# Kernel optimization log

Measured on AMD Instinct MI355X. Metric: run time of the kernel, lower is better.

The kernel has to match this reference:

```python
import jax, jax.numpy as jnp
import numpy as np

B, C, H, W = 8, 512, 32, 32


def setup_inputs() -> dict:
    key = jax.random.key(0)
    kx, kq, kk, k6 = jax.random.split(key, 4)
    std = 0.02
    return {
        "x": jax.random.normal(kx, (B, C, H, W), dtype=jnp.float32),
        "Wq": jax.random.normal(kq, (C, C), dtype=jnp.float32) * std,
        "bq": jnp.zeros((C,), dtype=jnp.float32),
        "Wk": jax.random.normal(kk, (C, C), dtype=jnp.float32) * std,
        "bk": jnp.zeros((C,), dtype=jnp.float32),
        "W6": jax.random.normal(k6, (C, C), dtype=jnp.float32) * std,
        "b6": jnp.zeros((C,), dtype=jnp.float32),
    }


def reference(x, Wq, bq, Wk, bk, W6, b6):
    b, c, h, w = x.shape
    hw = h * w
    scale = 1.0 / (c ** 0.5)
    # [B, HW, C] token-major view of the feature map
    xf = jnp.transpose(x.reshape(b, c, hw), (0, 2, 1))
    # 1x1 convs are per-pixel linear layers (weight layout: [C_out, C_in])
    q = xf @ Wq.T + bq                      # [B, HW, C]
    k = xf @ Wk.T + bk                      # [B, HW, C]
    # cross-batch attention scores: every pixel attends to every pixel of every image
    scores = q.reshape(b * hw, c) @ k.reshape(b * hw, c).T   # [B*HW, B*HW]
    s = scores.reshape(b * hw, b, hw)
    # per-query: max response within each image, then mean over images
    xw = jnp.max(s, axis=-1).mean(axis=-1)  # [B*HW]
    xw = xw.reshape(b, hw) * scale
    xw = jax.nn.softmax(xw, axis=-1).reshape(b, 1, h, w)
    x5 = x * xw                             # spatial gating
    # final 1x1 conv
    of = jnp.transpose(x5.reshape(b, c, hw), (0, 2, 1)) @ W6.T + b6
    return jnp.transpose(of, (0, 2, 1)).reshape(b, c, h, w)
```

## Files before the change

### kernel.cpp

```cpp
#include <hip/hip_runtime.h>


typedef __attribute__((ext_vector_type(8))) short bf16x8;
typedef __attribute__((ext_vector_type(4))) float f32x4;
typedef __attribute__((ext_vector_type(2))) long long i64x2;

__device__ __forceinline__ unsigned short f2bf(float f) {
  unsigned u = __builtin_bit_cast(unsigned, f);
  u += 0x7FFFu + ((u >> 16) & 1u);
  return (unsigned short)(u >> 16);
}

__device__ __forceinline__ unsigned char f2e4m3(float x) {
  unsigned u = __builtin_bit_cast(unsigned, x);
  unsigned char s = (unsigned char)((u >> 24) & 0x80u);
  unsigned a = u & 0x7FFFFFFFu;
  if (a >= 0x43E00000u) return s | 0x7Eu;
  if (a < 0x3C800000u) {
    float q = __builtin_bit_cast(float, a) * 512.f;
    int m = (int)(q + 0.5f);
    return s | (unsigned char)m;
  }
  unsigned r = a + 0x7FFFFu + ((a >> 20) & 1u);
  int e = (int)((r >> 23) & 0xFF) - 127;
  if (e > 8) return s | 0x7Eu;
  unsigned m3 = (r >> 20) & 0x7u;
  return s | (unsigned char)(((e + 7) << 3) | m3);
}

__device__ __forceinline__ void gload_lds16(const void* g, void* l) {
  __builtin_amdgcn_global_load_lds(
      (const __attribute__((address_space(1))) unsigned int*)g,
      (__attribute__((address_space(3))) unsigned int*)l, 16, 0, 0);
}

__global__ __launch_bounds__(256) void prep(const float* __restrict__ x,
                                            const float* __restrict__ Wq,
                                            const float* __restrict__ Wk,
                                            const float* __restrict__ W6,
                                            short* __restrict__ xt,
                                            short* __restrict__ wcat) {
  const int bid = blockIdx.x, u = threadIdx.x;
  if (bid < 1024) {
    const int p0 = (bid & 15) * 64, c0 = ((bid >> 4) & 7) * 64, b = bid >> 7;
    __shared__ float t[64][65];
    {
      const int p4 = u & 15, cr = u >> 4;
      for (int cc = 0; cc < 4; ++cc) {
        const int c = cc * 16 + cr;
        const float4 v = *(const float4*)&x[((size_t)(b * 512 + c0 + c)) * 1024 + p0 + p4 * 4];
        t[p4 * 4 + 0][c] = v.x; t[p4 * 4 + 1][c] = v.y;
        t[p4 * 4 + 2][c] = v.z; t[p4 * 4 + 3][c] = v.w;
      }
    }
    __syncthreads();
    {
      const int c4 = u & 15, pr = u >> 4;
      for (int pp = 0; pp < 4; ++pp) {
        const int p = pp * 16 + pr;
        ushort4 o;
        o.x = f2bf(t[p][c4 * 4 + 0]); o.y = f2bf(t[p][c4 * 4 + 1]);
        o.z = f2bf(t[p][c4 * 4 + 2]); o.w = f2bf(t[p][c4 * 4 + 3]);
        *(ushort4*)&xt[((size_t)(b * 1024 + p0 + p)) * 512 + c0 + c4 * 4] = o;
      }
    }
  } else {
    const int i = (bid - 1024) * 256 + u;
    const int idx = i * 4;
    const float* src = (idx < 262144) ? Wq : (idx < 524288) ? Wk : W6;
    const float4 v = *(const float4*)&src[idx & 262143];
    ushort4 o;
    o.x = f2bf(v.x); o.y = f2bf(v.y); o.z = f2bf(v.z); o.w = f2bf(v.w);
    *(ushort4*)&wcat[idx] = o;
  }
}

__global__ __launch_bounds__(256) void gemm_qk(const short* __restrict__ xt,
                                               const short* __restrict__ wcat,
                                               const float* __restrict__ bq,
                                               const float* __restrict__ bk,
                                               unsigned char* __restrict__ qk8) {
  __shared__ short lds_a[128 * 64];
  __shared__ short lds_b[128 * 64];
  const int tid = threadIdx.x, w = tid >> 6, lane = tid & 63;
  const int wr = w >> 1, wc = w & 1;
  const int quad = lane >> 4, lcol = lane & 15;
  const int srow = lane & 15, skq = lane >> 4;
  const int m0 = blockIdx.x * 128, n0 = blockIdx.y * 128;

  f32x4 acc[4][4];
#pragma unroll
  for (int i = 0; i < 4; ++i)
#pragma unroll
    for (int j = 0; j < 4; ++j)
#pragma unroll
      for (int r = 0; r < 4; ++r) acc[i][j][r] = 0.f;

  const short* Abase = xt + (size_t)(m0 + srow) * 512 + skq * 8;
  const short* Bbase = wcat + (size_t)(n0 + srow) * 512 + skq * 8;

  for (int kt = 0; kt < 8; ++kt) {
    const int kb = kt * 64;
    __syncthreads();
#pragma unroll
    for (int gg = 0; gg < 2; ++gg) {
      const int g = w + gg * 4;
      gload_lds16(Abase + (size_t)(g * 16) * 512 + kb,      lds_a + g * 1024);
      gload_lds16(Abase + (size_t)(g * 16) * 512 + kb + 32, lds_a + g * 1024 + 512);
      gload_lds16(Bbase + (size_t)(g * 16) * 512 + kb,      lds_b + g * 1024);
      gload_lds16(Bbase + (size_t)(g * 16) * 512 + kb + 32, lds_b + g * 1024 + 512);
    }
    __syncthreads();
#pragma unroll
    for (int h = 0; h < 2; ++h) {
      bf16x8 af[4], bf[4];
#pragma unroll
      for (int i = 0; i < 4; ++i)
        af[i] = *(const bf16x8*)&lds_a[(wr * 4 + i) * 1024 + h * 512 + lane * 8];
#pragma unroll
      for (int j = 0; j < 4; ++j)
        bf[j] = *(const bf16x8*)&lds_b[(wc * 4 + j) * 1024 + h * 512 + lane * 8];
#pragma unroll
      for (int i = 0; i < 4; ++i)
#pragma unroll
        for (int j = 0; j < 4; ++j)
          acc[i][j] = __builtin_amdgcn_mfma_f32_16x16x32_bf16(af[i], bf[j], acc[i][j], 0, 0, 0);
    }
  }

  const float* bias = (blockIdx.y >= 4) ? bk : bq;
#pragma unroll
  for (int i = 0; i < 4; ++i)
#pragma unroll
    for (int j = 0; j < 4; ++j) {
      const int row = m0 + wr * 64 + i * 16 + quad * 4;
      const int col = n0 + wc * 64 + j * 16 + lcol;
      const float bv = bias[col & 511];
#pragma unroll
      for (int r = 0; r < 4; ++r)
        qk8[(size_t)(row + r) * 1024 + col] = f2e4m3(acc[i][j][r] + bv);
    }
}

__global__ __launch_bounds__(256) void gemm_scores(const unsigned char* __restrict__ qk8,
                                                   float* __restrict__ wsmx) {
  __shared__ unsigned char lds_a[8192];
  __shared__ unsigned char lds_b[8192];
  __shared__ float partial[128][2];
  const int tid = threadIdx.x, w = tid >> 6, lane = tid & 63;
  const int wr = w >> 1, wc = w & 1;
  const int quad = lane >> 4, lcol = lane & 15;
  const int skq = lane >> 4, srow = lane & 15;
  const int m0 = blockIdx.x * 128, n0 = blockIdx.y * 128;

  f32x4 acc[4][4];
#pragma unroll
  for (int i = 0; i < 4; ++i)
#pragma unroll
    for (int j = 0; j < 4; ++j)
#pragma unroll
      for (int r = 0; r < 4; ++r) acc[i][j][r] = 0.f;

  const unsigned char* Abase = qk8 + (size_t)(m0 + srow) * 1024 + skq * 16;
  const unsigned char* Bbase = qk8 + (size_t)(n0 + srow) * 1024 + 512 + skq * 16;

  for (int kt = 0; kt < 8; ++kt) {
    const int kb = kt * 64;
    __syncthreads();
    gload_lds16(Abase + (size_t)(w * 16) * 1024 + kb,       lds_a + w * 1024);
    gload_lds16(Abase + (size_t)((4 + w) * 16) * 1024 + kb, lds_a + (4 + w) * 1024);
    gload_lds16(Bbase + (size_t)(w * 16) * 1024 + kb,       lds_b + w * 1024);
    gload_lds16(Bbase + (size_t)((4 + w) * 16) * 1024 + kb, lds_b + (4 + w) * 1024);
    __syncthreads();
    i64x2 af[4], bf[4];
#pragma unroll
    for (int i = 0; i < 4; ++i) af[i] = *(const i64x2*)&lds_a[(wr * 4 + i) * 1024 + lane * 16];
#pragma unroll
    for (int j = 0; j < 4; ++j) bf[j] = *(const i64x2*)&lds_b[(wc * 4 + j) * 1024 + lane * 16];
#pragma unroll
    for (int i = 0; i < 4; ++i)
#pragma unroll
      for (int j = 0; j < 4; ++j) {
        acc[i][j] = __builtin_amdgcn_mfma_f32_16x16x32_fp8_fp8(af[i].x, bf[j].x, acc[i][j], 0, 0, 0);
        acc[i][j] = __builtin_amdgcn_mfma_f32_16x16x32_fp8_fp8(af[i].y, bf[j].y, acc[i][j], 0, 0, 0);
      }
  }

#pragma unroll
  for (int i = 0; i < 4; ++i) {
#pragma unroll
    for (int r = 0; r < 4; ++r) {
      float v = fmaxf(fmaxf(acc[i][0][r], acc[i][1][r]),
                      fmaxf(acc[i][2][r], acc[i][3][r]));
#pragma unroll
      for (int off = 1; off < 16; off <<= 1) v = fmaxf(v, __shfl_xor(v, off));
      if (lcol == 0) partial[wr * 64 + i * 16 + quad * 4 + r][wc] = v;
    }
  }
  __syncthreads();
  if (tid < 128)
    wsmx[(size_t)blockIdx.y * 8192 + m0 + tid] = fmaxf(partial[tid][0], partial[tid][1]);
}

__global__ __launch_bounds__(1024) void softmax_xw(const float* __restrict__ wsmx,
                                                   float* __restrict__ xw) {
  const int b = blockIdx.x, p = threadIdx.x;
  const int m = b * 1024 + p;
  float s = 0.f;
#pragma unroll
  for (int img = 0; img < 8; ++img) {
    float mx = -1e30f;
#pragma unroll
    for (int t = 0; t < 8; ++t) mx = fmaxf(mx, wsmx[(size_t)(img * 8 + t) * 8192 + m]);
    s += mx;
  }
  const float logit = s * 0.005524271728019903f;
  __shared__ float red[16];
  float v = logit;
#pragma unroll
  for (int off = 32; off >= 1; off >>= 1) v = fmaxf(v, __shfl_xor(v, off));
  if ((p & 63) == 0) red[p >> 6] = v;
  __syncthreads();
  float bmax = red[0];
#pragma unroll
  for (int t = 1; t < 16; ++t) bmax = fmaxf(bmax, red[t]);
  const float e = expf(logit - bmax);
  float sv = e;
#pragma unroll
  for (int off = 32; off >= 1; off >>= 1) sv += __shfl_xor(sv, off);
  __syncthreads();
  if ((p & 63) == 0) red[p >> 6] = sv;
  __syncthreads();
  float bsum = 0.f;
#pragma unroll
  for (int t = 0; t < 16; ++t) bsum += red[t];
  xw[m] = e / bsum;
}

__global__ __launch_bounds__(256) void gemm_out(const short* __restrict__ xt,
                                                const short* __restrict__ wcat,
                                                const float* __restrict__ xw,
                                                const float* __restrict__ b6,
                                                float* __restrict__ out) {
  __shared__ short lds_a[64 * 64];
  __shared__ short lds_b[64 * 64];
  const int tid = threadIdx.x, w = tid >> 6, lane = tid & 63;
  const int wr = w >> 1, wc = w & 1;
  const int quad = lane >> 4, lcol = lane & 15;
  const int srow = lane & 15, skq = lane >> 4;
  const int m0 = blockIdx.x * 64, n0 = blockIdx.y * 64;

  f32x4 acc[2][2];
#pragma unroll
  for (int i = 0; i < 2; ++i)
#pragma unroll
    for (int j = 0; j < 2; ++j)
#pragma unroll
      for (int r = 0; r < 4; ++r) acc[i][j][r] = 0.f;

  const short* Abase = xt + (size_t)(m0 + w * 16 + srow) * 512 + skq * 8;
  const short* Bbase = wcat + (size_t)(1024 + n0 + w * 16 + srow) * 512 + skq * 8;

  for (int kt = 0; kt < 8; ++kt) {
    const int kb = kt * 64;
    __syncthreads();
    gload_lds16(Abase + kb,      lds_a + w * 1024);
    gload_lds16(Abase + kb + 32, lds_a + w * 1024 + 512);
    gload_lds16(Bbase + kb,      lds_b + w * 1024);
    gload_lds16(Bbase + kb + 32, lds_b + w * 1024 + 512);
    __syncthreads();
#pragma unroll
    for (int h = 0; h < 2; ++h) {
      bf16x8 af[2], bf[2];
#pragma unroll
      for (int i = 0; i < 2; ++i)
        af[i] = *(const bf16x8*)&lds_a[(wr * 2 + i) * 1024 + h * 512 + lane * 8];
#pragma unroll
      for (int j = 0; j < 2; ++j)
        bf[j] = *(const bf16x8*)&lds_b[(wc * 2 + j) * 1024 + h * 512 + lane * 8];
#pragma unroll
      for (int i = 0; i < 2; ++i)
#pragma unroll
        for (int j = 0; j < 2; ++j)
          acc[i][j] = __builtin_amdgcn_mfma_f32_16x16x32_bf16(af[i], bf[j], acc[i][j], 0, 0, 0);
    }
  }

#pragma unroll
  for (int i = 0; i < 2; ++i) {
    const int mbase = m0 + wr * 32 + i * 16 + quad * 4;
    const int b = mbase >> 10, p = mbase & 1023;
    const float4 wv = *(const float4*)&xw[mbase];
#pragma unroll
    for (int j = 0; j < 2; ++j) {
      const int col = n0 + wc * 32 + j * 16 + lcol;
      const float bias = b6[col];
      float4 o;
      o.x = acc[i][j][0] * wv.x + bias;
      o.y = acc[i][j][1] * wv.y + bias;
      o.z = acc[i][j][2] * wv.z + bias;
      o.w = acc[i][j][3] * wv.w + bias;
      *(float4*)&out[((size_t)(b * 512 + col)) * 1024 + p] = o;
    }
  }
}

extern "C" void kernel_launch(void* const* d_in, const int* in_sizes, int n_in,
                              void* d_out, int out_size, void* d_ws, size_t ws_size,
                              hipStream_t stream) {
  const float* x  = (const float*)d_in[0];
  const float* Wq = (const float*)d_in[1];
  const float* bq = (const float*)d_in[2];
  const float* Wk = (const float*)d_in[3];
  const float* bk = (const float*)d_in[4];
  const float* W6 = (const float*)d_in[5];
  const float* b6 = (const float*)d_in[6];
  float* out = (float*)d_out;

  char* ws = (char*)d_ws;
  short* xt          = (short*)(ws + 0);
  short* wcat        = (short*)(ws + 8388608);
  unsigned char* qk8 = (unsigned char*)(ws + 10485760);
  float* wsmx        = (float*)(ws + 18874368);
  float* xw          = (float*)(ws + 20971520);

  prep<<<1792, 256, 0, stream>>>(x, Wq, Wk, W6, xt, wcat);
  gemm_qk<<<dim3(64, 8), 256, 0, stream>>>(xt, wcat, bq, bk, qk8);
  gemm_scores<<<dim3(64, 64), 256, 0, stream>>>(qk8, wsmx);
  softmax_xw<<<8, 1024, 0, stream>>>(wsmx, xw);
  gemm_out<<<dim3(128, 8), 256, 0, stream>>>(xt, wcat, xw, b6, out);
}
```

Before: 194.5 us.

## Restructure score GEMM: per-wave 32-row strips, A in registers, larger K chunks

The FP8 score GEMM now gives each wave a full 32x128 strip instead of a 2x2 wave grid. A fragments are loaded straight from global memory into registers, and B is staged through LDS in two 256-byte K halves rather than eight 64-byte steps. This cuts the barrier count and drops the LDS partial-max reduction, since each wave writes its row maxima directly. In exchange it uses a larger LDS buffer (32KB) and more accumulator registers, which may lower occupancy, and the A loads from global are uncoalesced per-lane 16-byte reads.

```diff
diff --git a/kernel.cpp b/kernel.cpp
--- a/kernel.cpp
+++ b/kernel.cpp
@@ -144,62 +144,70 @@
 
 __global__ __launch_bounds__(256) void gemm_scores(const unsigned char* __restrict__ qk8,
                                                    float* __restrict__ wsmx) {
-  __shared__ unsigned char lds_a[8192];
-  __shared__ unsigned char lds_b[8192];
-  __shared__ float partial[128][2];
+  __shared__ unsigned char lds_b[32768];
   const int tid = threadIdx.x, w = tid >> 6, lane = tid & 63;
-  const int wr = w >> 1, wc = w & 1;
   const int quad = lane >> 4, lcol = lane & 15;
-  const int skq = lane >> 4, srow = lane & 15;
+  const int srow = lane & 15, skb = (lane >> 4) * 16;
   const int m0 = blockIdx.x * 128, n0 = blockIdx.y * 128;
 
-  f32x4 acc[4][4];
-#pragma unroll
-  for (int i = 0; i < 4; ++i)
-#pragma unroll
-    for (int j = 0; j < 4; ++j)
-#pragma unroll
-      for (int r = 0; r < 4; ++r) acc[i][j][r] = 0.f;
-
-  const unsigned char* Abase = qk8 + (size_t)(m0 + srow) * 1024 + skq * 16;
-  const unsigned char* Bbase = qk8 + (size_t)(n0 + srow) * 1024 + 512 + skq * 16;
-
-  for (int kt = 0; kt < 8; ++kt) {
-    const int kb = kt * 64;
-    __syncthreads();
-    gload_lds16(Abase + (size_t)(w * 16) * 1024 + kb,       lds_a + w * 1024);
-    gload_lds16(Abase + (size_t)((4 + w) * 16) * 1024 + kb, lds_a + (4 + w) * 1024);
-    gload_lds16(Bbase + (size_t)(w * 16) * 1024 + kb,       lds_b + w * 1024);
-    gload_lds16(Bbase + (size_t)((4 + w) * 16) * 1024 + kb, lds_b + (4 + w) * 1024);
-    __syncthreads();
-    i64x2 af[4], bf[4];
-#pragma unroll
-    for (int i = 0; i < 4; ++i) af[i] = *(const i64x2*)&lds_a[(wr * 4 + i) * 1024 + lane * 16];
-#pragma unroll
-    for (int j = 0; j < 4; ++j) bf[j] = *(const i64x2*)&lds_b[(wc * 4 + j) * 1024 + lane * 16];
-#pragma unroll
-    for (int i = 0; i < 4; ++i)
-#pragma unroll
-      for (int j = 0; j < 4; ++j) {
-        acc[i][j] = __builtin_amdgcn_mfma_f32_16x16x32_fp8_fp8(af[i].x, bf[j].x, acc[i][j], 0, 0, 0);
-        acc[i][j] = __builtin_amdgcn_mfma_f32_16x16x32_fp8_fp8(af[i].y, bf[j].y, acc[i][j], 0, 0, 0);
+  f32x4 acc[2][8];
+#pragma unroll
+  for (int rg = 0; rg < 2; ++rg)
+#pragma unroll
+    for (int j = 0; j < 8; ++j)
+#pragma unroll
+      for (int r = 0; r < 4; ++r) acc[rg][j][r] = 0.f;
+
+  const unsigned char* Abase = qk8 + (size_t)(m0 + w * 32 + srow) * 1024 + skb;
+  const unsigned char* Bbase = qk8 + (size_t)(n0 + srow) * 1024 + 512 + skb;
+
+#pragma unroll
+  for (int kh = 0; kh < 2; ++kh) {
+    __syncthreads();
+#pragma unroll
+    for (int jj = 0; jj < 2; ++jj) {
+      const int j = w * 2 + jj;
+#pragma unroll
+      for (int kb = 0; kb < 4; ++kb)
+        gload_lds16(Bbase + (size_t)(j * 16) * 1024 + kh * 256 + kb * 64,
+                    lds_b + j * 4096 + kb * 1024);
+    }
+    i64x2 af[2][4];
+#pragma unroll
+    for (int rg = 0; rg < 2; ++rg)
+#pragma unroll
+      for (int kb = 0; kb < 4; ++kb)
+        af[rg][kb] = *(const i64x2*)(Abase + (size_t)rg * 16384 + kh * 256 + kb * 64);
+    __syncthreads();
+#pragma unroll
+    for (int kb = 0; kb < 4; ++kb) {
+#pragma unroll
+      for (int j = 0; j < 8; ++j) {
+        const i64x2 bf = *(const i64x2*)&lds_b[j * 4096 + kb * 1024 + lane * 16];
+#pragma unroll
+        for (int rg = 0; rg < 2; ++rg) {
+          acc[rg][j] = __builtin_amdgcn_mfma_f32_16x16x32_fp8_fp8(
+              af[rg][kb].x, bf.x, acc[rg][j], 0, 0, 0);
+          acc[rg][j] = __builtin_amdgcn_mfma_f32_16x16x32_fp8_fp8(
+              af[rg][kb].y, bf.y, acc[rg][j], 0, 0, 0);
+        }
       }
-  }
-
-#pragma unroll
-  for (int i = 0; i < 4; ++i) {
+    }
+  }
+
+#pragma unroll
+  for (int rg = 0; rg < 2; ++rg) {
 #pragma unroll
     for (int r = 0; r < 4; ++r) {
-      float v = fmaxf(fmaxf(acc[i][0][r], acc[i][1][r]),
-                      fmaxf(acc[i][2][r], acc[i][3][r]));
+      float v = acc[rg][0][r];
+#pragma unroll
+      for (int j = 1; j < 8; ++j) v = fmaxf(v, acc[rg][j][r]);
 #pragma unroll
       for (int off = 1; off < 16; off <<= 1) v = fmaxf(v, __shfl_xor(v, off));
-      if (lcol == 0) partial[wr * 64 + i * 16 + quad * 4 + r][wc] = v;
-    }
-  }
-  __syncthreads();
-  if (tid < 128)
-    wsmx[(size_t)blockIdx.y * 8192 + m0 + tid] = fmaxf(partial[tid][0], partial[tid][1]);
+      if (lcol == 0)
+        wsmx[(size_t)blockIdx.y * 8192 + m0 + w * 32 + rg * 16 + quad * 4 + r] = v;
+    }
+  }
 }
 
 __global__ __launch_bounds__(1024) void softmax_xw(const float* __restrict__ wsmx,
```

New measurement: 191.6 us. Within noise of the previous version (-1.5%).
